# Kernel optimization log

Hardware: AMD Instinct MI355X
Metric: run time of the kernel (lower is better)

## Reference

```python
import jax, jax.numpy as jnp
import numpy as np

GROUPS = 16
EPS = 1e-5


def _dcn_v2(x, offset, mask, weight):
    """Modulated deformable 3x3 conv, stride=1, pad=1, no bias.
    x: [B,C,H,W], offset: [B,18,H,W] (dy,dx interleaved per kernel point),
    mask: [B,9,H,W] (modulation scalars), weight: [O,C,3,3]."""
    B, C, H, W = x.shape
    O = weight.shape[0]
    K = 9
    # kernel-point displacements, row-major (kh, kw): k = kh*3 + kw
    ky = jnp.repeat(jnp.arange(3) - 1, 3).astype(x.dtype)   # [9]
    kx = jnp.tile(jnp.arange(3) - 1, 3).astype(x.dtype)      # [9]
    dy = offset[:, 0::2]  # [B,9,H,W]
    dx = offset[:, 1::2]  # [B,9,H,W]
    hh = jnp.arange(H, dtype=x.dtype)
    ww = jnp.arange(W, dtype=x.dtype)
    # sampling coordinates (stride=1, pad=1)
    ys = hh[None, None, :, None] + ky[None, :, None, None] + dy  # [B,9,H,W]
    xs = ww[None, None, None, :] + kx[None, :, None, None] + dx  # [B,9,H,W]

    y0 = jnp.floor(ys)
    x0 = jnp.floor(xs)
    wy1 = ys - y0
    wx1 = xs - x0
    y0i = y0.astype(jnp.int32)
    x0i = x0.astype(jnp.int32)

    flat = x.reshape(B, C, H * W)

    def gather(yi, xi, w):
        # yi, xi, w: [B,9,H,W]; zero-padding outside the image
        valid = (yi >= 0) & (yi < H) & (xi >= 0) & (xi < W)
        idx = jnp.clip(yi, 0, H - 1) * W + jnp.clip(xi, 0, W - 1)  # [B,9,H,W]
        g = jnp.take_along_axis(flat, idx.reshape(B, 1, K * H * W), axis=2)
        g = g.reshape(B, C, K, H, W)
        return g * (w * valid.astype(x.dtype))[:, None]  # [B,C,9,H,W]

    val = (gather(y0i,     x0i,     (1 - wy1) * (1 - wx1))
         + gather(y0i,     x0i + 1, (1 - wy1) * wx1)
         + gather(y0i + 1, x0i,     wy1 * (1 - wx1))
         + gather(y0i + 1, x0i + 1, wy1 * wx1))
    val = val * mask[:, None]  # modulation
    # implicit GEMM: [B,C,9,H,W] x [O,C,9] -> [B,O,H,W]
    return jnp.einsum('bckhw,ock->bohw', val, weight.reshape(O, C, K))


def _group_norm(x, gamma, beta):
    B, C, H, W = x.shape
    xg = x.reshape(B, GROUPS, C // GROUPS, H, W)
    mu = xg.mean(axis=(2, 3, 4), keepdims=True)
    var = xg.var(axis=(2, 3, 4), keepdims=True)
    xn = ((xg - mu) * jax.lax.rsqrt(var + EPS)).reshape(B, C, H, W)
    return xn * gamma[None, :, None, None] + beta[None, :, None, None]


def setup_inputs() -> dict:
    key = jax.random.key(0)
    k1, k2, k3, k4 = jax.random.split(key, 4)
    B, C, O, H, W = 8, 256, 256, 64, 64
    x = jax.random.normal(k1, (B, C, H, W), dtype=jnp.float32)
    offset = jax.random.normal(k2, (B, 18, H, W), dtype=jnp.float32)
    mask = jax.random.uniform(k3, (B, 9, H, W), dtype=jnp.float32)
    weight = jax.random.normal(k4, (O, C, 3, 3), dtype=jnp.float32) * (1.0 / np.sqrt(C * 9))
    gamma = jnp.ones((O,), dtype=jnp.float32)
    beta = jnp.zeros((O,), dtype=jnp.float32)
    return {"x": x, "offset": offset, "mask": mask, "weight": weight,
            "gamma": gamma, "beta": beta}


def reference(x, offset, mask, weight, gamma, beta):
    out = _dcn_v2(x, offset, mask, weight)
    return _group_norm(out, gamma, beta)
```

## Files before the change

### kernel.cpp

```cpp
#include <hip/hip_runtime.h>
#include <stdint.h>


#define B_ 8
#define C_ 256
#define O_ 256
#define H_ 64
#define W_ 64
#define HW_ 4096
#define KTOT 2304
#define GROUPS_ 16
#define EPS_ 1e-5f
#define NSTEP 36
#define VROW 72

typedef float  f32x4  __attribute__((ext_vector_type(4)));
typedef short  short8 __attribute__((ext_vector_type(8)));
typedef unsigned int   u32;
typedef unsigned short u16;

#define XT_BYTES   (B_*HW_*C_*2)
#define WIMG_OFF   XT_BYTES
#define WIMG_BYTES (72*16*64*16)
#define STATS_OFF  (WIMG_OFF + WIMG_BYTES)

__device__ __forceinline__ u32 bf16r(float f) {
    u32 u = __float_as_uint(f);
    return (u + 0x7fffu + ((u >> 16) & 1u)) >> 16;
}
__device__ __forceinline__ u32 pack_bf16x2(float lo, float hi) {
    return bf16r(lo) | (bf16r(hi) << 16);
}
__device__ __forceinline__ u32 pack_perm(float lo, float hi) {
    return __builtin_amdgcn_perm(__float_as_uint(hi), __float_as_uint(lo), 0x07060302u);
}
__device__ __forceinline__ float bflo(u32 u) { return __uint_as_float(u << 16); }
__device__ __forceinline__ float bfhi_f(u32 u) { return __uint_as_float(u); }

__device__ __forceinline__ void barrier_lds() {
    asm volatile("s_waitcnt lgkmcnt(0)\n\ts_barrier" ::: "memory");
}

__global__ void k_prep(const float* __restrict__ x, u16* __restrict__ xt,
                       const float* __restrict__ w, u16* __restrict__ wimg,
                       float* __restrict__ stats) {
    const int bid = blockIdx.x;
    const int tid = threadIdx.x;
    if (bid >= 2048 + 288) {
        stats[tid] = 0.f;
        return;
    }
    if (bid < 2048) {
        __shared__ float tile[64][65];
        const int b = bid >> 8, ct = (bid >> 6) & 3, pt = bid & 63;
#pragma unroll
        for (int pass = 0; pass < 4; ++pass) {
            const int r  = (tid >> 4) + pass * 16;
            const int pq = tid & 15;
            const f32x4 v = *(const f32x4*)&x[(((size_t)(b * C_ + ct * 64 + r)) << 12)
                                              + pt * 64 + pq * 4];
            tile[r][pq * 4 + 0] = v.x;
            tile[r][pq * 4 + 1] = v.y;
            tile[r][pq * 4 + 2] = v.z;
            tile[r][pq * 4 + 3] = v.w;
        }
        __syncthreads();
        const int pr = tid >> 2, cg = tid & 3;
        u32 o[8];
#pragma unroll
        for (int j = 0; j < 8; ++j)
            o[j] = pack_bf16x2(tile[cg * 16 + 2 * j][pr], tile[cg * 16 + 2 * j + 1][pr]);
        u16* dst = &xt[(((size_t)b << 12) + pt * 64 + pr) * 256 + ct * 64 + cg * 16];
        *(uint4*)dst       = *(uint4*)&o[0];
        *(uint4*)(dst + 8) = *(uint4*)&o[4];
    } else {
        const int item = (bid - 2048) * 256 + tid;
        if (item < 72 * 1024) {
            const int sub = item >> 10;
            const int idx = item & 1023;
            const int k  = sub >> 3;
            const int c0 = (sub & 7) * 32;
            const int lane = idx & 63;
            const int frag = idx >> 6;
            const int col = lane & 15, quad = lane >> 4;
            const int n = frag * 16 + col;
            const float* src = w + (size_t)n * KTOT + (size_t)(c0 + quad * 8) * 9 + k;
            u32 o[4];
#pragma unroll
            for (int j = 0; j < 4; ++j)
                o[j] = pack_bf16x2(src[(size_t)(2 * j) * 9], src[(size_t)(2 * j + 1) * 9]);
            *(uint4*)&wimg[((size_t)sub * 1024 + idx) * 8] = *(uint4*)o;
        }
    }
}

__device__ __forceinline__ void issue_gather(const u16* __restrict__ cb,
                                             const float* __restrict__ mwp,
                                             const int* __restrict__ mip,
                                             int gpos, uint4 g[4], f32x4& mw) {
    mw = *(const f32x4*)&mwp[gpos * 4];
    const int4 ix = *(const int4*)&mip[gpos * 4];
    g[0] = *(const uint4*)(cb + ix.x);
    g[1] = *(const uint4*)(cb + ix.y);
    g[2] = *(const uint4*)(cb + ix.z);
    g[3] = *(const uint4*)(cb + ix.w);
}

__device__ __forceinline__ void interp_store(const uint4 g[4], f32x4 mw, u16* dst) {
    float s[8];
#pragma unroll
    for (int i = 0; i < 8; ++i) s[i] = 0.f;
    const float ww[4] = {mw.x, mw.y, mw.z, mw.w};
#pragma unroll
    for (int cr = 0; cr < 4; ++cr) {
        const float wg = ww[cr];
        const uint4 a = g[cr];
        s[0] += wg * bflo(a.x);  s[1] += wg * bfhi_f(a.x);
        s[2] += wg * bflo(a.y);  s[3] += wg * bfhi_f(a.y);
        s[4] += wg * bflo(a.z);  s[5] += wg * bfhi_f(a.z);
        s[6] += wg * bflo(a.w);  s[7] += wg * bfhi_f(a.w);
    }
    uint4 pk;
    pk.x = pack_perm(s[0], s[1]);
    pk.y = pack_perm(s[2], s[3]);
    pk.z = pack_perm(s[4], s[5]);
    pk.w = pack_perm(s[6], s[7]);
    *(uint4*)dst = pk;
}

__device__ __forceinline__ void load_wfrags(const u16* __restrict__ wimg, int s,
                                            int wid, int lane, short8 bf[4]) {
#pragma unroll
    for (int kc = 0; kc < 2; ++kc)
#pragma unroll
        for (int ni = 0; ni < 2; ++ni)
            bf[kc * 2 + ni] = *(const short8*)
                &wimg[(((size_t)(2 * s + kc) * 16 + wid * 2 + ni) * 64 + lane) * 8];
}

__launch_bounds__(512, 4)
__global__ void k_dcn(const u16* __restrict__ xt, const u16* __restrict__ wimg,
                      const float* __restrict__ offp, const float* __restrict__ mskp,
                      float* __restrict__ out, float* __restrict__ stats) {
    __shared__ __align__(16) float meta_w[9 * 64 * 4];
    __shared__ __align__(16) int   meta_i[9 * 64 * 4];
    __shared__ __align__(16) u16   lds_v[2][64 * VROW];

    const int tid = threadIdx.x;
    const int gid = blockIdx.x;
    const int b   = gid & 7;
    const int m0  = (gid >> 3) * 64;
    const int lane = tid & 63, wid = tid >> 6;
    const int col = lane & 15, quad = lane >> 4;
    const int gpos = tid >> 3, slot = tid & 7;

    const u16* xtb = xt + ((size_t)b << 20);

    for (int it = tid; it < 576; it += 512) {
        const int pos = it & 63, k = it >> 6;
        const int pg = m0 + pos;
        const int hh = pg >> 6, wwi = pg & 63;
        const float dy = offp[((size_t)(b * 18 + 2 * k) << 12) + pg];
        const float dx = offp[((size_t)(b * 18 + 2 * k + 1) << 12) + pg];
        const float mv = mskp[((size_t)(b * 9 + k) << 12) + pg];
        const float ys = (float)(hh + (k / 3) - 1) + dy;
        const float xs = (float)(wwi + (k % 3) - 1) + dx;
        const float y0f = floorf(ys), x0f = floorf(xs);
        const int y0 = (int)y0f, x0 = (int)x0f;
        const float wy1 = ys - y0f, wx1 = xs - x0f;
        const float wy0 = 1.f - wy1, wx0 = 1.f - wx1;
        const int y1 = y0 + 1, x1 = x0 + 1;
        const float vy0 = (y0 >= 0 && y0 < H_) ? 1.f : 0.f;
        const float vy1 = (y1 >= 0 && y1 < H_) ? 1.f : 0.f;
        const float vx0 = (x0 >= 0 && x0 < W_) ? 1.f : 0.f;
        const float vx1 = (x1 >= 0 && x1 < W_) ? 1.f : 0.f;
        const int y0c = min(max(y0, 0), H_ - 1), y1c = min(max(y1, 0), H_ - 1);
        const int x0c = min(max(x0, 0), W_ - 1), x1c = min(max(x1, 0), W_ - 1);
        meta_w[it * 4 + 0] = mv * wy0 * wx0 * vy0 * vx0;
        meta_w[it * 4 + 1] = mv * wy0 * wx1 * vy0 * vx1;
        meta_w[it * 4 + 2] = mv * wy1 * wx0 * vy1 * vx0;
        meta_w[it * 4 + 3] = mv * wy1 * wx1 * vy1 * vx1;
        meta_i[it * 4 + 0] = (y0c * W_ + x0c) << 8;
        meta_i[it * 4 + 1] = (y0c * W_ + x1c) << 8;
        meta_i[it * 4 + 2] = (y1c * W_ + x0c) << 8;
        meta_i[it * 4 + 3] = (y1c * W_ + x1c) << 8;
    }
    __syncthreads();

    uint4 g2[2][4]; f32x4 mw2[2]; short8 bf[4];
    issue_gather(xtb + 0 + slot * 8, &meta_w[0], &meta_i[0], gpos, g2[0], mw2[0]);
    interp_store(g2[0], mw2[0], &lds_v[0][gpos * VROW + slot * 8]);
    issue_gather(xtb + 64 + slot * 8, &meta_w[0], &meta_i[0], gpos, g2[1], mw2[1]);
    __syncthreads();

    f32x4 acc[4][2];
#pragma unroll
    for (int i = 0; i < 4; ++i)
#pragma unroll
        for (int j = 0; j < 2; ++j) acc[i][j] = (f32x4){0.f, 0.f, 0.f, 0.f};

#pragma unroll 2
    for (int s = 0; s < NSTEP; ++s) {
        const int p = s & 1;

        load_wfrags(wimg, s, wid, lane, bf);

        if (s + 2 < NSTEP) {
            const int sn = s + 2;
            const int kn = sn >> 2, c0n = (sn & 3) * 64;
            issue_gather(xtb + c0n + slot * 8, &meta_w[kn * 256], &meta_i[kn * 256],
                         gpos, g2[p], mw2[p]);
        }

#pragma unroll
        for (int kc = 0; kc < 2; ++kc) {
            short8 af[4];
#pragma unroll
            for (int mi = 0; mi < 4; ++mi)
                af[mi] = *(const short8*)
                    &lds_v[p][(mi * 16 + col) * VROW + kc * 32 + quad * 8];
#pragma unroll
            for (int mi = 0; mi < 4; ++mi)
#pragma unroll
                for (int ni = 0; ni < 2; ++ni)
                    acc[mi][ni] = __builtin_amdgcn_mfma_f32_16x16x32_bf16(
                        af[mi], bf[kc * 2 + ni], acc[mi][ni], 0, 0, 0);
        }

        if (s + 1 < NSTEP)
            interp_store(g2[1 - p], mw2[1 - p], &lds_v[1 - p][gpos * VROW + slot * 8]);

        barrier_lds();
    }

#pragma unroll
    for (int mi = 0; mi < 4; ++mi)
#pragma unroll
        for (int ni = 0; ni < 2; ++ni) {
            const int o  = wid * 32 + ni * 16 + col;
            const int pg = m0 + mi * 16 + quad * 4;
            *(f32x4*)(out + (((size_t)b * O_ + o) << 12) + pg) = acc[mi][ni];
        }

#pragma unroll
    for (int ni = 0; ni < 2; ++ni) {
        float s = 0.f, s2 = 0.f;
#pragma unroll
        for (int mi = 0; mi < 4; ++mi) {
            f32x4 v = acc[mi][ni];
            s  += v.x + v.y + v.z + v.w;
            s2 += v.x * v.x + v.y * v.y + v.z * v.z + v.w * v.w;
        }
#pragma unroll
        for (int d = 32; d > 0; d >>= 1) {
            s  += __shfl_xor(s, d, 64);
            s2 += __shfl_xor(s2, d, 64);
        }
        if (lane == 0) {
            const int gI = wid * 2 + ni;
            atomicAdd(&stats[b * GROUPS_ + gI], s);
            atomicAdd(&stats[128 + b * GROUPS_ + gI], s2);
        }
    }
}

__global__ void k_gn(float* __restrict__ out, const float* __restrict__ stats,
                     const float* __restrict__ gamma, const float* __restrict__ beta) {
    const int blk = blockIdx.x;
    const int b = blk >> 8, o = blk & 255;
    const int gI = b * GROUPS_ + (o >> 4);
    const float n = 65536.f;
    const float mean = stats[gI] / n;
    const float var  = stats[128 + gI] / n - mean * mean;
    const float inv  = rsqrtf(fmaxf(var, 0.f) + EPS_);
    const float scale = inv * gamma[o];
    const float shift = beta[o] - mean * scale;
    f32x4* p = (f32x4*)(out + ((size_t)blk << 12));
    const int t = threadIdx.x;
#pragma unroll
    for (int i = 0; i < 4; ++i) {
        f32x4 v = p[t + i * 256];
        p[t + i * 256] = v * scale + shift;
    }
}

extern "C" void kernel_launch(void* const* d_in, const int* in_sizes, int n_in,
                              void* d_out, int out_size, void* d_ws, size_t ws_size,
                              hipStream_t stream) {
    const float* x     = (const float*)d_in[0];
    const float* offp  = (const float*)d_in[1];
    const float* mskp  = (const float*)d_in[2];
    const float* w     = (const float*)d_in[3];
    const float* gamma = (const float*)d_in[4];
    const float* beta  = (const float*)d_in[5];
    float* outp = (float*)d_out;

    u16*   xt    = (u16*)d_ws;
    u16*   wimg  = (u16*)((char*)d_ws + WIMG_OFF);
    float* stats = (float*)((char*)d_ws + STATS_OFF);

    k_prep<<<dim3(2048 + 288 + 1), dim3(256), 0, stream>>>(x, xt, w, wimg, stats);
    k_dcn<<<dim3(512), dim3(512), 0, stream>>>(xt, wimg, offp, mskp, outp, stats);
    k_gn<<<dim3(2048), dim3(256), 0, stream>>>(outp, stats, gamma, beta);
}
```

Measured before the change: 181.2 us.

## Shrink DCN tiles to 32 pixels with 4 waves and fragment-order LDS

The fused deformable-conv GEMM kernel now uses blocks of 256 threads covering 32 output pixels instead of 512 threads covering 64, which doubles the grid to 1024 blocks. Each wave now computes 64 output channels over 32 pixels. The bilinear-gathered values are written into LDS already in MFMA A-fragment order, so the A loads become contiguous without row padding. The gather prefetch distance drops from two steps to one, and metadata is reloaded only when the kernel point changes. This aims to improve occupancy and load balance and to cut LDS bank conflicts. In exchange, weight fragments are reused across fewer pixels, so per-step weight loads double relative to the MFMA work, and the shallower prefetch exposes more gather latency.

```diff
diff --git a/kernel.cpp b/kernel.cpp
--- a/kernel.cpp
+++ b/kernel.cpp
@@ -12,7 +12,6 @@
 #define GROUPS_ 16
 #define EPS_ 1e-5f
 #define NSTEP 36
-#define VROW 72
 
 typedef float  f32x4  __attribute__((ext_vector_type(4)));
 typedef short  short8 __attribute__((ext_vector_type(8)));
@@ -94,18 +93,6 @@
     }
 }
 
-__device__ __forceinline__ void issue_gather(const u16* __restrict__ cb,
-                                             const float* __restrict__ mwp,
-                                             const int* __restrict__ mip,
-                                             int gpos, uint4 g[4], f32x4& mw) {
-    mw = *(const f32x4*)&mwp[gpos * 4];
-    const int4 ix = *(const int4*)&mip[gpos * 4];
-    g[0] = *(const uint4*)(cb + ix.x);
-    g[1] = *(const uint4*)(cb + ix.y);
-    g[2] = *(const uint4*)(cb + ix.z);
-    g[3] = *(const uint4*)(cb + ix.w);
-}
-
 __device__ __forceinline__ void interp_store(const uint4 g[4], f32x4 mw, u16* dst) {
     float s[8];
 #pragma unroll
@@ -128,36 +115,26 @@
     *(uint4*)dst = pk;
 }
 
-__device__ __forceinline__ void load_wfrags(const u16* __restrict__ wimg, int s,
-                                            int wid, int lane, short8 bf[4]) {
-#pragma unroll
-    for (int kc = 0; kc < 2; ++kc)
-#pragma unroll
-        for (int ni = 0; ni < 2; ++ni)
-            bf[kc * 2 + ni] = *(const short8*)
-                &wimg[(((size_t)(2 * s + kc) * 16 + wid * 2 + ni) * 64 + lane) * 8];
-}
-
-__launch_bounds__(512, 4)
+__launch_bounds__(256, 4)
 __global__ void k_dcn(const u16* __restrict__ xt, const u16* __restrict__ wimg,
                       const float* __restrict__ offp, const float* __restrict__ mskp,
                       float* __restrict__ out, float* __restrict__ stats) {
-    __shared__ __align__(16) float meta_w[9 * 64 * 4];
-    __shared__ __align__(16) int   meta_i[9 * 64 * 4];
-    __shared__ __align__(16) u16   lds_v[2][64 * VROW];
+    __shared__ __align__(16) float meta_w[9 * 32 * 4];
+    __shared__ __align__(16) int   meta_i[9 * 32 * 4];
+    __shared__ __align__(16) u16   lds_v[2][4 * 512];
 
     const int tid = threadIdx.x;
     const int gid = blockIdx.x;
     const int b   = gid & 7;
-    const int m0  = (gid >> 3) * 64;
+    const int m0  = (gid >> 3) * 32;
     const int lane = tid & 63, wid = tid >> 6;
     const int col = lane & 15, quad = lane >> 4;
     const int gpos = tid >> 3, slot = tid & 7;
 
     const u16* xtb = xt + ((size_t)b << 20);
 
-    for (int it = tid; it < 576; it += 512) {
-        const int pos = it & 63, k = it >> 6;
+    for (int it = tid; it < 288; it += 256) {
+        const int pos = it & 31, k = it >> 5;
         const int pg = m0 + pos;
         const int hh = pg >> 6, wwi = pg & 63;
         const float dy = offp[((size_t)(b * 18 + 2 * k) << 12) + pg];
@@ -187,78 +164,102 @@
     }
     __syncthreads();
 
-    uint4 g2[2][4]; f32x4 mw2[2]; short8 bf[4];
-    issue_gather(xtb + 0 + slot * 8, &meta_w[0], &meta_i[0], gpos, g2[0], mw2[0]);
-    interp_store(g2[0], mw2[0], &lds_v[0][gpos * VROW + slot * 8]);
-    issue_gather(xtb + 64 + slot * 8, &meta_w[0], &meta_i[0], gpos, g2[1], mw2[1]);
+    const int woff = (((gpos >> 4) * 2 + (slot >> 2)) * 64
+                      + (slot & 3) * 16 + (gpos & 15)) * 8;
+    const u16* gbase = xtb + slot * 8;
+
+    f32x4 mwc = *(const f32x4*)&meta_w[gpos * 4];
+    int4  ixc = *(const int4*)&meta_i[gpos * 4];
+
+    uint4 g[4];
+    {
+        const u16* cb = gbase;
+        g[0] = *(const uint4*)(cb + ixc.x);
+        g[1] = *(const uint4*)(cb + ixc.y);
+        g[2] = *(const uint4*)(cb + ixc.z);
+        g[3] = *(const uint4*)(cb + ixc.w);
+        interp_store(g, mwc, &lds_v[0][woff]);
+    }
     __syncthreads();
 
-    f32x4 acc[4][2];
-#pragma unroll
-    for (int i = 0; i < 4; ++i)
-#pragma unroll
-        for (int j = 0; j < 2; ++j) acc[i][j] = (f32x4){0.f, 0.f, 0.f, 0.f};
+    f32x4 acc[2][4];
+#pragma unroll
+    for (int i = 0; i < 2; ++i)
+#pragma unroll
+        for (int j = 0; j < 4; ++j) acc[i][j] = (f32x4){0.f, 0.f, 0.f, 0.f};
 
 #pragma unroll 2
     for (int s = 0; s < NSTEP; ++s) {
         const int p = s & 1;
 
-        load_wfrags(wimg, s, wid, lane, bf);
-
-        if (s + 2 < NSTEP) {
-            const int sn = s + 2;
-            const int kn = sn >> 2, c0n = (sn & 3) * 64;
-            issue_gather(xtb + c0n + slot * 8, &meta_w[kn * 256], &meta_i[kn * 256],
-                         gpos, g2[p], mw2[p]);
-        }
-
+        short8 bf[8];
+#pragma unroll
+        for (int kc = 0; kc < 2; ++kc)
+#pragma unroll
+            for (int ni = 0; ni < 4; ++ni)
+                bf[kc * 4 + ni] = *(const short8*)
+                    &wimg[(((size_t)(2 * s + kc) * 16 + wid * 4 + ni) * 64 + lane) * 8];
+
+        if (s + 1 < NSTEP) {
+            const int sn = s + 1;
+            if ((sn & 3) == 0) {
+                mwc = *(const f32x4*)&meta_w[((sn >> 2) * 32 + gpos) * 4];
+                ixc = *(const int4*)&meta_i[((sn >> 2) * 32 + gpos) * 4];
+            }
+            const u16* cb = gbase + (sn & 3) * 64;
+            g[0] = *(const uint4*)(cb + ixc.x);
+            g[1] = *(const uint4*)(cb + ixc.y);
+            g[2] = *(const uint4*)(cb + ixc.z);
+            g[3] = *(const uint4*)(cb + ixc.w);
+        }
+
+        const u16* vb = &lds_v[p][lane * 8];
 #pragma unroll
         for (int kc = 0; kc < 2; ++kc) {
-            short8 af[4];
-#pragma unroll
-            for (int mi = 0; mi < 4; ++mi)
-                af[mi] = *(const short8*)
-                    &lds_v[p][(mi * 16 + col) * VROW + kc * 32 + quad * 8];
-#pragma unroll
-            for (int mi = 0; mi < 4; ++mi)
-#pragma unroll
-                for (int ni = 0; ni < 2; ++ni)
+            short8 af[2];
+#pragma unroll
+            for (int mi = 0; mi < 2; ++mi)
+                af[mi] = *(const short8*)&vb[(mi * 2 + kc) * 512];
+#pragma unroll
+            for (int mi = 0; mi < 2; ++mi)
+#pragma unroll
+                for (int ni = 0; ni < 4; ++ni)
                     acc[mi][ni] = __builtin_amdgcn_mfma_f32_16x16x32_bf16(
-                        af[mi], bf[kc * 2 + ni], acc[mi][ni], 0, 0, 0);
+                        af[mi], bf[kc * 4 + ni], acc[mi][ni], 0, 0, 0);
         }
 
         if (s + 1 < NSTEP)
-            interp_store(g2[1 - p], mw2[1 - p], &lds_v[1 - p][gpos * VROW + slot * 8]);
+            interp_store(g, mwc, &lds_v[1 - p][woff]);
 
         barrier_lds();
     }
 
 #pragma unroll
-    for (int mi = 0; mi < 4; ++mi)
-#pragma unroll
-        for (int ni = 0; ni < 2; ++ni) {
-            const int o  = wid * 32 + ni * 16 + col;
+    for (int mi = 0; mi < 2; ++mi)
+#pragma unroll
+        for (int ni = 0; ni < 4; ++ni) {
+            const int o  = wid * 64 + ni * 16 + col;
             const int pg = m0 + mi * 16 + quad * 4;
             *(f32x4*)(out + (((size_t)b * O_ + o) << 12) + pg) = acc[mi][ni];
         }
 
 #pragma unroll
-    for (int ni = 0; ni < 2; ++ni) {
-        float s = 0.f, s2 = 0.f;
-#pragma unroll
-        for (int mi = 0; mi < 4; ++mi) {
+    for (int ni = 0; ni < 4; ++ni) {
+        float s1 = 0.f, s2 = 0.f;
+#pragma unroll
+        for (int mi = 0; mi < 2; ++mi) {
             f32x4 v = acc[mi][ni];
-            s  += v.x + v.y + v.z + v.w;
+            s1 += v.x + v.y + v.z + v.w;
             s2 += v.x * v.x + v.y * v.y + v.z * v.z + v.w * v.w;
         }
 #pragma unroll
         for (int d = 32; d > 0; d >>= 1) {
-            s  += __shfl_xor(s, d, 64);
+            s1 += __shfl_xor(s1, d, 64);
             s2 += __shfl_xor(s2, d, 64);
         }
         if (lane == 0) {
-            const int gI = wid * 2 + ni;
-            atomicAdd(&stats[b * GROUPS_ + gI], s);
+            const int gI = wid * 4 + ni;
+            atomicAdd(&stats[b * GROUPS_ + gI], s1);
             atomicAdd(&stats[128 + b * GROUPS_ + gI], s2);
         }
     }
@@ -300,6 +301,6 @@
     float* stats = (float*)((char*)d_ws + STATS_OFF);
 
     k_prep<<<dim3(2048 + 288 + 1), dim3(256), 0, stream>>>(x, xt, w, wimg, stats);
-    k_dcn<<<dim3(512), dim3(512), 0, stream>>>(xt, wimg, offp, mskp, outp, stats);
+    k_dcn<<<dim3(1024), dim3(256), 0, stream>>>(xt, wimg, offp, mskp, outp, stats);
     k_gn<<<dim3(2048), dim3(256), 0, stream>>>(outp, stats, gamma, beta);
 }
```

Measured after the change: 233.4 us. 1.29x slower.

## Deepen DCN pipeline with four LDS buffers and prefetched weight fragments

Applied to the files above, without the earlier changes.

Expands the sampled-activation LDS ring from two to four buffers and raises the gather prefetch distance from two steps to three. Weight fragments are now double-buffered in registers, with the next step's fragments loaded during the current MFMA step. The block barrier now runs every other step instead of every step. This is meant to hide gather and weight-load latency and cut barrier stalls, at the cost of more LDS per block and more registers, which may lower the number of resident blocks.

```diff
diff --git a/kernel.cpp b/kernel.cpp
--- a/kernel.cpp
+++ b/kernel.cpp
@@ -144,7 +144,7 @@
                       float* __restrict__ out, float* __restrict__ stats) {
     __shared__ __align__(16) float meta_w[9 * 64 * 4];
     __shared__ __align__(16) int   meta_i[9 * 64 * 4];
-    __shared__ __align__(16) u16   lds_v[2][64 * VROW];
+    __shared__ __align__(16) u16   lds_v[4][64 * VROW];
 
     const int tid = threadIdx.x;
     const int gid = blockIdx.x;
@@ -187,10 +187,13 @@
     }
     __syncthreads();
 
-    uint4 g2[2][4]; f32x4 mw2[2]; short8 bf[4];
+    uint4 g2[2][4]; f32x4 mw2[2]; short8 bf_cur[4], bf_nxt[4];
     issue_gather(xtb + 0 + slot * 8, &meta_w[0], &meta_i[0], gpos, g2[0], mw2[0]);
+    issue_gather(xtb + 64 + slot * 8, &meta_w[0], &meta_i[0], gpos, g2[1], mw2[1]);
+    load_wfrags(wimg, 0, wid, lane, bf_cur);
     interp_store(g2[0], mw2[0], &lds_v[0][gpos * VROW + slot * 8]);
-    issue_gather(xtb + 64 + slot * 8, &meta_w[0], &meta_i[0], gpos, g2[1], mw2[1]);
+    interp_store(g2[1], mw2[1], &lds_v[1][gpos * VROW + slot * 8]);
+    issue_gather(xtb + 128 + slot * 8, &meta_w[0], &meta_i[0], gpos, g2[1], mw2[1]);
     __syncthreads();
 
     f32x4 acc[4][2];
@@ -199,17 +202,15 @@
 #pragma unroll
         for (int j = 0; j < 2; ++j) acc[i][j] = (f32x4){0.f, 0.f, 0.f, 0.f};
 
-#pragma unroll 2
+#pragma unroll 4
     for (int s = 0; s < NSTEP; ++s) {
-        const int p = s & 1;
-
-        load_wfrags(wimg, s, wid, lane, bf);
-
-        if (s + 2 < NSTEP) {
-            const int sn = s + 2;
-            const int kn = sn >> 2, c0n = (sn & 3) * 64;
-            issue_gather(xtb + c0n + slot * 8, &meta_w[kn * 256], &meta_i[kn * 256],
-                         gpos, g2[p], mw2[p]);
+        if (s + 1 < NSTEP) load_wfrags(wimg, s + 1, wid, lane, bf_nxt);
+
+        if (s + 3 < NSTEP) {
+            const int sn = s + 3;
+            issue_gather(xtb + (sn & 3) * 64 + slot * 8,
+                         &meta_w[(sn >> 2) * 256], &meta_i[(sn >> 2) * 256],
+                         gpos, g2[s & 1], mw2[s & 1]);
         }
 
 #pragma unroll
@@ -218,19 +219,25 @@
 #pragma unroll
             for (int mi = 0; mi < 4; ++mi)
                 af[mi] = *(const short8*)
-                    &lds_v[p][(mi * 16 + col) * VROW + kc * 32 + quad * 8];
+                    &lds_v[s & 3][(mi * 16 + col) * VROW + kc * 32 + quad * 8];
 #pragma unroll
             for (int mi = 0; mi < 4; ++mi)
 #pragma unroll
                 for (int ni = 0; ni < 2; ++ni)
                     acc[mi][ni] = __builtin_amdgcn_mfma_f32_16x16x32_bf16(
-                        af[mi], bf[kc * 2 + ni], acc[mi][ni], 0, 0, 0);
-        }
-
-        if (s + 1 < NSTEP)
-            interp_store(g2[1 - p], mw2[1 - p], &lds_v[1 - p][gpos * VROW + slot * 8]);
-
-        barrier_lds();
+                        af[mi], bf_cur[kc * 2 + ni], acc[mi][ni], 0, 0, 0);
+        }
+
+        if (s + 2 < NSTEP)
+            interp_store(g2[(s & 1) ^ 1], mw2[(s & 1) ^ 1],
+                         &lds_v[(s + 2) & 3][gpos * VROW + slot * 8]);
+
+        if (s & 1) barrier_lds();
+
+        if (s + 1 < NSTEP) {
+#pragma unroll
+            for (int j = 0; j < 4; ++j) bf_cur[j] = bf_nxt[j];
+        }
     }
 
 #pragma unroll
@@ -244,21 +251,21 @@
 
 #pragma unroll
     for (int ni = 0; ni < 2; ++ni) {
-        float s = 0.f, s2 = 0.f;
+        float s1 = 0.f, s2 = 0.f;
 #pragma unroll
         for (int mi = 0; mi < 4; ++mi) {
             f32x4 v = acc[mi][ni];
-            s  += v.x + v.y + v.z + v.w;
+            s1 += v.x + v.y + v.z + v.w;
             s2 += v.x * v.x + v.y * v.y + v.z * v.z + v.w * v.w;
         }
 #pragma unroll
         for (int d = 32; d > 0; d >>= 1) {
-            s  += __shfl_xor(s, d, 64);
+            s1 += __shfl_xor(s1, d, 64);
             s2 += __shfl_xor(s2, d, 64);
         }
         if (lane == 0) {
             const int gI = wid * 2 + ni;
-            atomicAdd(&stats[b * GROUPS_ + gI], s);
+            atomicAdd(&stats[b * GROUPS_ + gI], s1);
             atomicAdd(&stats[128 + b * GROUPS_ + gI], s2);
         }
     }
```

Result: slower. 195.9 us (+8.1%).

## Double M-tile to 128 positions and stage weights in LDS via async DMA

Applied to the files above, without the earlier changes.

Each block now covers 128 output positions with 1024 threads (16 waves split into two M halves and eight N slices), so each weight tile is shared by twice as many positions. Weight fragments are copied asynchronously into double-buffered LDS with global_load_lds instead of per-wave global loads, and explicit vmcnt waits sit before the barrier. Gather indices shrink to 16-bit in LDS and are shifted when used. The trade-offs are higher LDS use per block, fewer blocks (256), and more complex manual synchronisation.

```diff
diff --git a/kernel.cpp b/kernel.cpp
--- a/kernel.cpp
+++ b/kernel.cpp
@@ -13,6 +13,7 @@
 #define EPS_ 1e-5f
 #define NSTEP 36
 #define VROW 72
+#define BM 128
 
 typedef float  f32x4  __attribute__((ext_vector_type(4)));
 typedef short  short8 __attribute__((ext_vector_type(8)));
@@ -96,14 +97,14 @@
 
 __device__ __forceinline__ void issue_gather(const u16* __restrict__ cb,
                                              const float* __restrict__ mwp,
-                                             const int* __restrict__ mip,
+                                             const u16* __restrict__ mip,
                                              int gpos, uint4 g[4], f32x4& mw) {
     mw = *(const f32x4*)&mwp[gpos * 4];
-    const int4 ix = *(const int4*)&mip[gpos * 4];
-    g[0] = *(const uint4*)(cb + ix.x);
-    g[1] = *(const uint4*)(cb + ix.y);
-    g[2] = *(const uint4*)(cb + ix.z);
-    g[3] = *(const uint4*)(cb + ix.w);
+    const ushort4 ix = *(const ushort4*)&mip[gpos * 4];
+    g[0] = *(const uint4*)(cb + ((int)ix.x << 8));
+    g[1] = *(const uint4*)(cb + ((int)ix.y << 8));
+    g[2] = *(const uint4*)(cb + ((int)ix.z << 8));
+    g[3] = *(const uint4*)(cb + ((int)ix.w << 8));
 }
 
 __device__ __forceinline__ void interp_store(const uint4 g[4], f32x4 mw, u16* dst) {
@@ -128,36 +129,39 @@
     *(uint4*)dst = pk;
 }
 
-__device__ __forceinline__ void load_wfrags(const u16* __restrict__ wimg, int s,
-                                            int wid, int lane, short8 bf[4]) {
-#pragma unroll
-    for (int kc = 0; kc < 2; ++kc)
-#pragma unroll
-        for (int ni = 0; ni < 2; ++ni)
-            bf[kc * 2 + ni] = *(const short8*)
-                &wimg[(((size_t)(2 * s + kc) * 16 + wid * 2 + ni) * 64 + lane) * 8];
-}
-
-__launch_bounds__(512, 4)
+__device__ __forceinline__ void dma_weights(const u16* __restrict__ wimg, int s,
+                                            u16* wlds_buf, int wid, int lane) {
+    const u16* gsrc = wimg + (size_t)(2 * s) * 8192;
+#pragma unroll
+    for (int j = 0; j < 2; ++j) {
+        const int chunk = j * 16 + wid;
+        __builtin_amdgcn_global_load_lds((const u32*)(gsrc + chunk * 512 + lane * 8),
+                                         (u32*)(wlds_buf + chunk * 512), 16, 0, 0);
+    }
+}
+
+__launch_bounds__(1024, 4)
 __global__ void k_dcn(const u16* __restrict__ xt, const u16* __restrict__ wimg,
                       const float* __restrict__ offp, const float* __restrict__ mskp,
                       float* __restrict__ out, float* __restrict__ stats) {
-    __shared__ __align__(16) float meta_w[9 * 64 * 4];
-    __shared__ __align__(16) int   meta_i[9 * 64 * 4];
-    __shared__ __align__(16) u16   lds_v[2][64 * VROW];
+    __shared__ __align__(16) float meta_w[9 * BM * 4];
+    __shared__ __align__(16) u16   meta_i[9 * BM * 4];
+    __shared__ __align__(16) u16   lds_v[2][BM * VROW];
+    __shared__ __align__(16) u16   wlds[2][16384];
 
     const int tid = threadIdx.x;
     const int gid = blockIdx.x;
     const int b   = gid & 7;
-    const int m0  = (gid >> 3) * 64;
+    const int m0  = (gid >> 3) * BM;
     const int lane = tid & 63, wid = tid >> 6;
+    const int mh = wid >> 3, nw = wid & 7;
     const int col = lane & 15, quad = lane >> 4;
     const int gpos = tid >> 3, slot = tid & 7;
 
     const u16* xtb = xt + ((size_t)b << 20);
 
-    for (int it = tid; it < 576; it += 512) {
-        const int pos = it & 63, k = it >> 6;
+    for (int it = tid; it < 9 * BM; it += 1024) {
+        const int pos = it & (BM - 1), k = it >> 7;
         const int pg = m0 + pos;
         const int hh = pg >> 6, wwi = pg & 63;
         const float dy = offp[((size_t)(b * 18 + 2 * k) << 12) + pg];
@@ -180,17 +184,21 @@
         meta_w[it * 4 + 1] = mv * wy0 * wx1 * vy0 * vx1;
         meta_w[it * 4 + 2] = mv * wy1 * wx0 * vy1 * vx0;
         meta_w[it * 4 + 3] = mv * wy1 * wx1 * vy1 * vx1;
-        meta_i[it * 4 + 0] = (y0c * W_ + x0c) << 8;
-        meta_i[it * 4 + 1] = (y0c * W_ + x1c) << 8;
-        meta_i[it * 4 + 2] = (y1c * W_ + x0c) << 8;
-        meta_i[it * 4 + 3] = (y1c * W_ + x1c) << 8;
+        meta_i[it * 4 + 0] = (u16)(y0c * W_ + x0c);
+        meta_i[it * 4 + 1] = (u16)(y0c * W_ + x1c);
+        meta_i[it * 4 + 2] = (u16)(y1c * W_ + x0c);
+        meta_i[it * 4 + 3] = (u16)(y1c * W_ + x1c);
     }
     __syncthreads();
 
-    uint4 g2[2][4]; f32x4 mw2[2]; short8 bf[4];
+    uint4 g2[2][4]; f32x4 mw2[2];
+    dma_weights(wimg, 0, &wlds[0][0], wid, lane);
     issue_gather(xtb + 0 + slot * 8, &meta_w[0], &meta_i[0], gpos, g2[0], mw2[0]);
+    issue_gather(xtb + 64 + slot * 8, &meta_w[0], &meta_i[0], gpos, g2[1], mw2[1]);
     interp_store(g2[0], mw2[0], &lds_v[0][gpos * VROW + slot * 8]);
-    issue_gather(xtb + 64 + slot * 8, &meta_w[0], &meta_i[0], gpos, g2[1], mw2[1]);
+    __builtin_amdgcn_sched_barrier(0);
+    asm volatile("s_waitcnt vmcnt(4)" ::: "memory");
+    __builtin_amdgcn_sched_barrier(0);
     __syncthreads();
 
     f32x4 acc[4][2];
@@ -203,62 +211,74 @@
     for (int s = 0; s < NSTEP; ++s) {
         const int p = s & 1;
 
-        load_wfrags(wimg, s, wid, lane, bf);
+        if (s + 1 < NSTEP)
+            dma_weights(wimg, s + 1, &wlds[1 - p][0], wid, lane);
 
         if (s + 2 < NSTEP) {
             const int sn = s + 2;
-            const int kn = sn >> 2, c0n = (sn & 3) * 64;
-            issue_gather(xtb + c0n + slot * 8, &meta_w[kn * 256], &meta_i[kn * 256],
+            issue_gather(xtb + (sn & 3) * 64 + slot * 8,
+                         &meta_w[(sn >> 2) * (BM * 4)], &meta_i[(sn >> 2) * (BM * 4)],
                          gpos, g2[p], mw2[p]);
         }
 
 #pragma unroll
         for (int kc = 0; kc < 2; ++kc) {
+            short8 bf[2];
+#pragma unroll
+            for (int ni = 0; ni < 2; ++ni)
+                bf[ni] = *(const short8*)
+                    &wlds[p][kc * 8192 + (nw * 2 + ni) * 512 + lane * 8];
             short8 af[4];
 #pragma unroll
             for (int mi = 0; mi < 4; ++mi)
                 af[mi] = *(const short8*)
-                    &lds_v[p][(mi * 16 + col) * VROW + kc * 32 + quad * 8];
+                    &lds_v[p][(mh * 64 + mi * 16 + col) * VROW + kc * 32 + quad * 8];
 #pragma unroll
             for (int mi = 0; mi < 4; ++mi)
 #pragma unroll
                 for (int ni = 0; ni < 2; ++ni)
                     acc[mi][ni] = __builtin_amdgcn_mfma_f32_16x16x32_bf16(
-                        af[mi], bf[kc * 2 + ni], acc[mi][ni], 0, 0, 0);
+                        af[mi], bf[ni], acc[mi][ni], 0, 0, 0);
         }
 
         if (s + 1 < NSTEP)
             interp_store(g2[1 - p], mw2[1 - p], &lds_v[1 - p][gpos * VROW + slot * 8]);
 
-        barrier_lds();
+        if (s + 1 < NSTEP) {
+            __builtin_amdgcn_sched_barrier(0);
+            if (s + 2 < NSTEP) asm volatile("s_waitcnt vmcnt(4)" ::: "memory");
+            else               asm volatile("s_waitcnt vmcnt(0)" ::: "memory");
+            __builtin_amdgcn_sched_barrier(0);
+            barrier_lds();
+        }
     }
 
 #pragma unroll
     for (int mi = 0; mi < 4; ++mi)
 #pragma unroll
         for (int ni = 0; ni < 2; ++ni) {
-            const int o  = wid * 32 + ni * 16 + col;
-            const int pg = m0 + mi * 16 + quad * 4;
+            const int o  = nw * 32 + ni * 16 + col;
+            const int pg = m0 + mh * 64 + mi * 16 + quad * 4;
             *(f32x4*)(out + (((size_t)b * O_ + o) << 12) + pg) = acc[mi][ni];
         }
 
 #pragma unroll
     for (int ni = 0; ni < 2; ++ni) {
-        float s = 0.f, s2 = 0.f;
+        float s1 = 0.f, s2 = 0.f;
 #pragma unroll
         for (int mi = 0; mi < 4; ++mi) {
             f32x4 v = acc[mi][ni];
-            s  += v.x + v.y + v.z + v.w;
+            s1 += v.x + v.y + v.z + v.w;
             s2 += v.x * v.x + v.y * v.y + v.z * v.z + v.w * v.w;
         }
 #pragma unroll
         for (int d = 32; d > 0; d >>= 1) {
-            s  += __shfl_xor(s, d, 64);
+            s1 += __shfl_xor(s1, d, 64);
             s2 += __shfl_xor(s2, d, 64);
         }
         if (lane == 0) {
-            const int gI = wid * 2 + ni;
-            atomicAdd(&stats[b * GROUPS_ + gI], s);
+            const int gI = nw * 2 + ni;
+            atomicAdd(&stats[b * GROUPS_ + gI], s1);
             atomicAdd(&stats[128 + b * GROUPS_ + gI], s2);
         }
     }
@@ -300,6 +320,6 @@
     float* stats = (float*)((char*)d_ws + STATS_OFF);
 
     k_prep<<<dim3(2048 + 288 + 1), dim3(256), 0, stream>>>(x, xt, w, wimg, stats);
-    k_dcn<<<dim3(512), dim3(512), 0, stream>>>(xt, wimg, offp, mskp, outp, stats);
+    k_dcn<<<dim3(256), dim3(1024), 0, stream>>>(xt, wimg, offp, mskp, outp, stats);
     k_gn<<<dim3(2048), dim3(256), 0, stream>>>(outp, stats, gamma, beta);
 }
```

Result: slower. 188.6 us (+4.1%).
